# Kernel optimization log

Hardware: AMD Instinct MI355X
Metric: run time of the kernel (lower is better)

## Reference

```python
import jax, jax.numpy as jnp
import numpy as np

N, S, IN_F, TEXT_D, EMB, H = 128, 1024, 768, 512, 512, 8
HD = EMB // H  # 64


def setup_inputs() -> dict:
    key = jax.random.key(0)
    ks = jax.random.split(key, 14)
    sc = 0.02
    return {
        "v": jax.random.normal(ks[0], (1, N, 12, IN_F), dtype=jnp.float32),
        "t": jax.random.normal(ks[1], (N, S, TEXT_D), dtype=jnp.float32),
        "t_len": jax.random.randint(ks[2], (N,), 1, S + 1, dtype=jnp.int32),
        "W_fc1": jax.random.normal(ks[3], (EMB, IN_F), dtype=jnp.float32) * sc,
        "b_fc1": jnp.zeros((EMB,), jnp.float32),
        "W_fc2": jax.random.normal(ks[4], (EMB, 12 * EMB), dtype=jnp.float32) * sc,
        "b_fc2": jnp.zeros((EMB,), jnp.float32),
        "Wq": jax.random.normal(ks[5], (EMB, EMB), dtype=jnp.float32) * sc,
        "Wk": jax.random.normal(ks[6], (EMB, TEXT_D), dtype=jnp.float32) * sc,
        "Wv": jax.random.normal(ks[7], (EMB, TEXT_D), dtype=jnp.float32) * sc,
        "bq": jnp.zeros((EMB,), jnp.float32),
        "bk": jnp.zeros((EMB,), jnp.float32),
        "bv": jnp.zeros((EMB,), jnp.float32),
        "Wo": jax.random.normal(ks[8], (EMB, EMB), dtype=jnp.float32) * sc,
        "bo": jnp.zeros((EMB,), jnp.float32),
    }


def reference(v, t, t_len, W_fc1, b_fc1, W_fc2, b_fc2, Wq, Wk, Wv, bq, bk, bv, Wo, bo):
    # fc1 + ReLU: [1,N,12,IN_F] -> [N,12,EMB]
    x = jax.nn.relu(jnp.einsum('onif,ef->onie', v, W_fc1) + b_fc1)[0]
    # flatten + fc2 + ReLU -> [N, EMB]
    x = x.reshape(N, 12 * EMB)
    vfeat = jax.nn.relu(x @ W_fc2.T + b_fc2)
    # Batched ragged multihead attention, query length 1 per item.
    scale = 1.0 / jnp.sqrt(jnp.asarray(HD, vfeat.dtype))
    q = ((vfeat @ Wq.T + bq) * scale).reshape(N, H, HD)           # [N,H,HD]
    k = (jnp.einsum('nsd,ed->nse', t, Wk) + bk).reshape(N, S, H, HD)
    vv = (jnp.einsum('nsd,ed->nse', t, Wv) + bv).reshape(N, S, H, HD)
    scores = jnp.einsum('nhd,nshd->nhs', q, k)                    # [N,H,S]
    valid = (jnp.arange(S)[None, :] < t_len[:, None])[:, None, :]  # [N,1,S]
    scores = jnp.where(valid, scores, jnp.finfo(scores.dtype).min)
    w = jax.nn.softmax(scores, axis=-1)                           # [N,H,S]
    ctx = jnp.einsum('nhs,nshd->nhd', w, vv).reshape(N, EMB)
    attn_out = ctx @ Wo.T + bo                                    # [N,EMB]
    return vfeat, attn_out
```

## Files before the change

kernel.cpp:

```cpp
#include <hip/hip_runtime.h>

#define NB 128
#define SSEQ 1024
#define TD 512

typedef _Float16 half8 __attribute__((ext_vector_type(8)));
typedef _Float16 half4 __attribute__((ext_vector_type(4)));
typedef _Float16 half2v __attribute__((ext_vector_type(2)));
typedef float f32x4 __attribute__((ext_vector_type(4)));
typedef float f32x2 __attribute__((ext_vector_type(2)));

template<int AM, int BM>
__global__ __launch_bounds__(256) void k_gemm(
    const void* __restrict__ Av, int lda, long aSZ,
    const void* __restrict__ Bv, int ldb, long bSZ,
    const float* __restrict__ bias, const float* __restrict__ aRowScale,
    float scale, int doRelu, int outMode,
    float* __restrict__ outF, _Float16* __restrict__ outH,
    int ldc, int cColOff, int mtiles, int kTiles, long oSplit)
{
  __shared__ _Float16 As[64][72];
  __shared__ _Float16 Bs[64][72];
  int mt = blockIdx.x % mtiles, nt = blockIdx.x / mtiles;
  int sp = blockIdx.y, bz = blockIdx.z;
  int tid = threadIdx.x;
  int r = tid >> 2, kq = (tid & 3) * 16;
  int w = tid >> 6, l = tid & 63;
  long aoff = (long)bz * aSZ + (long)(mt * 64 + r) * lda + (long)sp * kTiles * 64 + kq;
  long boff = (long)bz * bSZ + (long)(nt * 64 + r) * ldb + (long)sp * kTiles * 64 + kq;
  const _Float16* apH = (const _Float16*)Av + aoff;
  const float*    apF = (const float*)Av + aoff;
  const _Float16* bpH = (const _Float16*)Bv + boff;
  const float*    bpF = (const float*)Bv + boff;
  float srA = 1.0f;
  if constexpr (AM == 2) srA = 1.0f / aRowScale[(mt * 64 + r) * 8 + bz];

  half8 pa0, pa1, pb0, pb1;
  f32x4 qa0, qa1, qa2, qa3, qc0, qc1, qc2, qc3;
  if constexpr (AM == 0) { pa0 = *(const half8*)apH; pa1 = *(const half8*)(apH + 8); }
  else { qa0 = *(const f32x4*)apF; qa1 = *(const f32x4*)(apF + 4);
         qa2 = *(const f32x4*)(apF + 8); qa3 = *(const f32x4*)(apF + 12); }
  if constexpr (BM == 0) { pb0 = *(const half8*)bpH; pb1 = *(const half8*)(bpH + 8); }
  else { qc0 = *(const f32x4*)bpF; qc1 = *(const f32x4*)(bpF + 4);
         qc2 = *(const f32x4*)(bpF + 8); qc3 = *(const f32x4*)(bpF + 12); }

  f32x4 acc[4];
  #pragma unroll
  for (int c = 0; c < 4; ++c) acc[c] = (f32x4){0.f, 0.f, 0.f, 0.f};
  int fr = l & 15, fo = (l >> 4) * 8;
  for (int kt = 0; kt < kTiles; ++kt) {
    __syncthreads();
    if constexpr (AM == 0) {
      *(half8*)&As[r][kq] = pa0; *(half8*)&As[r][kq + 8] = pa1;
    } else {
      f32x4 s0 = qa0, s1 = qa1, s2 = qa2, s3 = qa3;
      if constexpr (AM == 2) { s0 *= srA; s1 *= srA; s2 *= srA; s3 *= srA; }
      *(half4*)&As[r][kq + 0]  = __builtin_convertvector(s0, half4);
      *(half4*)&As[r][kq + 4]  = __builtin_convertvector(s1, half4);
      *(half4*)&As[r][kq + 8]  = __builtin_convertvector(s2, half4);
      *(half4*)&As[r][kq + 12] = __builtin_convertvector(s3, half4);
    }
    if constexpr (BM == 0) {
      *(half8*)&Bs[r][kq] = pb0; *(half8*)&Bs[r][kq + 8] = pb1;
    } else {
      *(half4*)&Bs[r][kq + 0]  = __builtin_convertvector(qc0, half4);
      *(half4*)&Bs[r][kq + 4]  = __builtin_convertvector(qc1, half4);
      *(half4*)&Bs[r][kq + 8]  = __builtin_convertvector(qc2, half4);
      *(half4*)&Bs[r][kq + 12] = __builtin_convertvector(qc3, half4);
    }
    __syncthreads();
    if (kt + 1 < kTiles) {
      apH += 64; apF += 64; bpH += 64; bpF += 64;
      if constexpr (AM == 0) { pa0 = *(const half8*)apH; pa1 = *(const half8*)(apH + 8); }
      else { qa0 = *(const f32x4*)apF; qa1 = *(const f32x4*)(apF + 4);
             qa2 = *(const f32x4*)(apF + 8); qa3 = *(const f32x4*)(apF + 12); }
      if constexpr (BM == 0) { pb0 = *(const half8*)bpH; pb1 = *(const half8*)(bpH + 8); }
      else { qc0 = *(const f32x4*)bpF; qc1 = *(const f32x4*)(bpF + 4);
             qc2 = *(const f32x4*)(bpF + 8); qc3 = *(const f32x4*)(bpF + 12); }
    }
    #pragma unroll
    for (int ks = 0; ks < 2; ++ks) {
      half8 af = *(const half8*)&As[16 * w + fr][ks * 32 + fo];
      #pragma unroll
      for (int c = 0; c < 4; ++c) {
        half8 bf = *(const half8*)&Bs[16 * c + fr][ks * 32 + fo];
        acc[c] = __builtin_amdgcn_mfma_f32_16x16x32_f16(af, bf, acc[c], 0, 0, 0);
      }
    }
  }
  int lrow = (l >> 4) * 4, lcol = l & 15;
  #pragma unroll
  for (int c = 0; c < 4; ++c) {
    #pragma unroll
    for (int rr = 0; rr < 4; ++rr) {
      int gm = mt * 64 + 16 * w + lrow + rr;
      int gn = nt * 64 + 16 * c + lcol;
      int ecol = gn + bz * cColOff;
      float vv = acc[c][rr];
      if (bias) vv += bias[ecol];
      vv *= scale;
      if (doRelu) vv = fmaxf(vv, 0.f);
      long oidx = (long)gm * ldc + ecol;
      if (outMode == 0) outF[oidx] = vv;
      else if (outMode == 1) outH[oidx] = (_Float16)vv;
      else outF[oidx + (long)sp * oSplit] = vv;
    }
  }
}

__global__ __launch_bounds__(256) void k_vfeat(
    const float* __restrict__ vacc, const float* __restrict__ b2,
    float* __restrict__ outF, _Float16* __restrict__ vf16)
{
  int i = blockIdx.x * 256 + threadIdx.x;
  float vv = b2[i & 511];
  #pragma unroll
  for (int sp = 0; sp < 16; ++sp) vv += vacc[sp * 65536 + i];
  vv = fmaxf(vv, 0.f);
  outF[i] = vv;
  vf16[i] = (_Float16)vv;
}

__global__ __launch_bounds__(256) void k_qk(
    const float* __restrict__ qf, const float* __restrict__ Wk,
    const float* __restrict__ bk, _Float16* __restrict__ qk16, float* __restrict__ qb)
{
  int n = blockIdx.x, tid = threadIdx.x;
  __shared__ float qs[512];
  qs[tid] = qf[n * 512 + tid];
  qs[tid + 256] = qf[n * 512 + tid + 256];
  __syncthreads();
  _Float16* qn = qk16 + (long)n * 8192;
  #pragma unroll 1
  for (int h = 0; h < 8; ++h) {
    float a0 = 0.f, a1 = 0.f;
    #pragma unroll 8
    for (int j = 0; j < 64; ++j) {
      float qv = qs[h * 64 + j];
      const float* wr = Wk + (long)(h * 64 + j) * 512;
      a0 = fmaf(qv, wr[tid], a0);
      a1 = fmaf(qv, wr[tid + 256], a1);
    }
    qn[h * 512 + tid] = (_Float16)a0;
    qn[h * 512 + tid + 256] = (_Float16)a1;
  }
  #pragma unroll
  for (int h = 8; h < 16; ++h) {
    qn[h * 512 + tid] = (_Float16)0.f;
    qn[h * 512 + tid + 256] = (_Float16)0.f;
  }
  if (tid < 64) {
    #pragma unroll 1
    for (int h = 0; h < 8; ++h) {
      float pb = qs[h * 64 + tid] * bk[h * 64 + tid];
      #pragma unroll
      for (int m = 1; m < 64; m <<= 1) pb += __shfl_xor(pb, m, 64);
      if (tid == 0) qb[n * 8 + h] = pb;
    }
  }
}

__global__ __launch_bounds__(256) void k_attn(
    const float* __restrict__ t, const int* __restrict__ tlen,
    const _Float16* __restrict__ qk16, const float* __restrict__ qb,
    float* __restrict__ pu, float* __restrict__ pl)
{
  int n = blockIdx.x >> 5, j = blockIdx.x & 31;
  int len = tlen[n];
  int base = j * 32;
  if (base >= len) return;
  int s1 = base + 32; if (s1 > len) s1 = len;
  int tid = threadIdx.x, wid = tid >> 6, l = tid & 63;

  __shared__ __align__(16) _Float16 ts[32][520];
  __shared__ __align__(16) float ws[32][8];
  __shared__ float lred[8];
  if (tid < 8) lred[tid] = 0.f;

  const float* tn = t + (long)n * SSEQ * TD;
  {
    f32x4 a0, a1, b0, b1;
    auto ld = [&](int c, f32x4& x0, f32x4& x1) {
      int sg = base + c * 4 + wid;
      if (sg < s1) {
        const float* p = tn + (long)sg * TD;
        x0 = *(const f32x4*)(p + 4 * l);
        x1 = *(const f32x4*)(p + 256 + 4 * l);
      } else {
        x0 = (f32x4){0.f,0.f,0.f,0.f}; x1 = (f32x4){0.f,0.f,0.f,0.f};
      }
    };
    ld(0, a0, a1); ld(1, b0, b1);
    #pragma unroll
    for (int c = 0; c < 8; c += 2) {
      half4 h0 = __builtin_convertvector(a0, half4);
      half4 h1 = __builtin_convertvector(a1, half4);
      int row = c * 4 + wid;
      if (c + 2 < 8) ld(c + 2, a0, a1);
      *(half4*)&ts[row][4 * l] = h0;
      *(half4*)&ts[row][256 + 4 * l] = h1;
      half4 g0 = __builtin_convertvector(b0, half4);
      half4 g1 = __builtin_convertvector(b1, half4);
      int row2 = c * 4 + 4 + wid;
      if (c + 3 < 8) ld(c + 3, b0, b1);
      *(half4*)&ts[row2][4 * l] = g0;
      *(half4*)&ts[row2][256 + 4 * l] = g1;
    }
  }
  __syncthreads();
  int fr = l & 15, fo = (l >> 4) * 8;
  if (wid < 2) {
    const _Float16* qn = qk16 + (long)n * 8192 + fr * 512 + fo;
    f32x4 acc = (f32x4){0.f, 0.f, 0.f, 0.f};
    #pragma unroll 4
    for (int kt = 0; kt < 16; ++kt) {
      half8 bf = *(const half8*)(qn + kt * 32);
      half8 af = *(const half8*)&ts[16 * wid + fr][kt * 32 + fo];
      acc = __builtin_amdgcn_mfma_f32_16x16x32_f16(af, bf, acc, 0, 0, 0);
    }
    float qbr = (fr < 8) ? qb[n * 8 + fr] : 0.f;
    float lac = 0.f;
    #pragma unroll
    for (int r = 0; r < 4; ++r) {
      int sl = 16 * wid + (l >> 4) * 4 + r;
      float wv = 0.f;
      if (fr < 8 && base + sl < s1) wv = __expf(acc[r] + qbr);
      if (fr < 8) ws[sl][fr] = wv;
      lac += wv;
    }
    if (fr < 8) atomicAdd(&lred[fr], lac);
  }
  __syncthreads();
  int col0 = 128 * wid + 2 * l;
  f32x2 u[8];
  #pragma unroll
  for (int h = 0; h < 8; ++h) u[h] = (f32x2){0.f, 0.f};
  #pragma unroll 4
  for (int r = 0; r < 32; ++r) {
    f32x4 wa = *(const f32x4*)&ws[r][0];
    f32x4 wb = *(const f32x4*)&ws[r][4];
    half2v tv = *(const half2v*)&ts[r][col0];
    f32x2 tp = { (float)tv[0], (float)tv[1] };
    u[0] += wa[0] * tp; u[1] += wa[1] * tp;
    u[2] += wa[2] * tp; u[3] += wa[3] * tp;
    u[4] += wb[0] * tp; u[5] += wb[1] * tp;
    u[6] += wb[2] * tp; u[7] += wb[3] * tp;
  }
  float* pn = pu + (long)n * 4096;
  #pragma unroll
  for (int h = 0; h < 8; ++h) {
    atomicAdd(&pn[h * 512 + col0], u[h][0]);
    atomicAdd(&pn[h * 512 + col0 + 1], u[h][1]);
  }
  if (tid < 8) atomicAdd(&pl[n * 8 + tid], lred[tid]);
}

extern "C" void kernel_launch(void* const* d_in, const int* in_sizes, int n_in,
                              void* d_out, int out_size, void* d_ws, size_t ws_size,
                              hipStream_t stream)
{
  const float* v    = (const float*)d_in[0];
  const float* t    = (const float*)d_in[1];
  const int*   tlen = (const int*)d_in[2];
  const float* W1   = (const float*)d_in[3];
  const float* b1   = (const float*)d_in[4];
  const float* W2   = (const float*)d_in[5];
  const float* b2   = (const float*)d_in[6];
  const float* Wq   = (const float*)d_in[7];
  const float* Wk   = (const float*)d_in[8];
  const float* Wv   = (const float*)d_in[9];
  const float* bq   = (const float*)d_in[10];
  const float* bk   = (const float*)d_in[11];
  const float* bv   = (const float*)d_in[12];
  const float* Wo   = (const float*)d_in[13];
  const float* bo   = (const float*)d_in[14];
  float* out = (float*)d_out;

  _Float16* hb   = (_Float16*)d_ws;
  _Float16* x16  = hb;
  _Float16* vf16 = hb + 786432l;
  _Float16* ctx16= hb + 851968l;
  _Float16* qk16 = hb + 917504l;
  float* fb   = (float*)(hb + 1966080l);
  float* vacc = fb;
  float* qf   = fb + 1048576l;
  float* pu   = fb + 1114112l;
  float* pl   = fb + 1638400l;
  float* qb   = fb + 1639424l;

  hipMemsetAsync(pu, 0, (524288l + 1024l) * sizeof(float), stream);
  k_gemm<1,1><<<dim3(192, 1, 1), 256, 0, stream>>>(v, 768, 0, W1, 768, 0,
      b1, nullptr, 1.f, 1, 1, nullptr, x16, 512, 0, 24, 12, 0);
  k_gemm<0,1><<<dim3(16, 16, 1), 256, 0, stream>>>(x16, 6144, 0, W2, 6144, 0,
      nullptr, nullptr, 1.f, 0, 2, vacc, nullptr, 512, 0, 2, 6, 65536);
  k_vfeat<<<256, 256, 0, stream>>>(vacc, b2, out, vf16);
  k_gemm<0,1><<<dim3(16, 1, 1), 256, 0, stream>>>(vf16, 512, 0, Wq, 512, 0,
      bq, nullptr, 0.125f, 0, 0, qf, nullptr, 512, 0, 2, 8, 0);
  k_qk<<<128, 256, 0, stream>>>(qf, Wk, bk, qk16, qb);
  k_attn<<<NB * 32, 256, 0, stream>>>(t, tlen, qk16, qb, pu, pl);
  k_gemm<2,1><<<dim3(2, 1, 8), 256, 0, stream>>>(pu, 4096, 512, Wv, 512, 32768,
      bv, pl, 1.f, 0, 1, nullptr, ctx16, 512, 64, 2, 8, 0);
  k_gemm<0,1><<<dim3(16, 1, 1), 256, 0, stream>>>(ctx16, 512, 0, Wo, 512, 0,
      bo, nullptr, 1.f, 0, 0, out + 65536, nullptr, 512, 0, 2, 8, 0);
}
```

Measured before the change: 518.9 us.

## Use MFMA for weighted-sum in attention and process two chunks per block

The attention kernel now handles 64 sequence positions per block in two 32-row sub-chunks, keeping per-block partial sums in registers across both chunks. The scalar FMA accumulation of exp-weights times text rows is replaced with a 16x16x32 f16 MFMA, with the weights stored as fp16 in a transposed shared buffer. This halves the global atomic flushes per sequence position and moves the weighted-sum work onto matrix cores. The trade-offs are fewer blocks, an extra barrier per chunk, strided column gathers from shared memory to build the B fragments, and lower precision because the weights are stored in fp16.

```diff
diff --git a/kernel.cpp b/kernel.cpp
--- a/kernel.cpp
+++ b/kernel.cpp
@@ -6,9 +6,7 @@
 
 typedef _Float16 half8 __attribute__((ext_vector_type(8)));
 typedef _Float16 half4 __attribute__((ext_vector_type(4)));
-typedef _Float16 half2v __attribute__((ext_vector_type(2)));
 typedef float f32x4 __attribute__((ext_vector_type(4)));
-typedef float f32x2 __attribute__((ext_vector_type(2)));
 
 template<int AM, int BM>
 __global__ __launch_bounds__(256) void k_gemm(
@@ -165,92 +163,103 @@
     const _Float16* __restrict__ qk16, const float* __restrict__ qb,
     float* __restrict__ pu, float* __restrict__ pl)
 {
-  int n = blockIdx.x >> 5, j = blockIdx.x & 31;
+  int n = blockIdx.x >> 4, j = blockIdx.x & 15;
   int len = tlen[n];
-  int base = j * 32;
-  if (base >= len) return;
-  int s1 = base + 32; if (s1 > len) s1 = len;
+  int base0 = j * 64;
+  if (base0 >= len) return;
   int tid = threadIdx.x, wid = tid >> 6, l = tid & 63;
+  int fr = l & 15, fo = (l >> 4) * 8;
 
   __shared__ __align__(16) _Float16 ts[32][520];
-  __shared__ __align__(16) float ws[32][8];
+  __shared__ __align__(16) _Float16 wst[16][32];
   __shared__ float lred[8];
   if (tid < 8) lred[tid] = 0.f;
 
   const float* tn = t + (long)n * SSEQ * TD;
-  {
-    f32x4 a0, a1, b0, b1;
-    auto ld = [&](int c, f32x4& x0, f32x4& x1) {
-      int sg = base + c * 4 + wid;
-      if (sg < s1) {
-        const float* p = tn + (long)sg * TD;
-        x0 = *(const f32x4*)(p + 4 * l);
-        x1 = *(const f32x4*)(p + 256 + 4 * l);
-      } else {
-        x0 = (f32x4){0.f,0.f,0.f,0.f}; x1 = (f32x4){0.f,0.f,0.f,0.f};
-      }
-    };
-    ld(0, a0, a1); ld(1, b0, b1);
+  const _Float16* qn = qk16 + (long)n * 8192 + fr * 512 + fo;
+  float qbr = (fr < 8) ? qb[n * 8 + fr] : 0.f;
+
+  f32x4 upv[8];
+  #pragma unroll
+  for (int dt = 0; dt < 8; ++dt) upv[dt] = (f32x4){0.f, 0.f, 0.f, 0.f};
+
+  #pragma unroll 1
+  for (int sub = 0; sub < 2; ++sub) {
+    int base = base0 + sub * 32;
+    if (base >= len) break;
+    int s1 = base + 32; if (s1 > len) s1 = len;
+    __syncthreads();
+    {
+      f32x4 a0, a1, b0, b1;
+      auto ld = [&](int c, f32x4& x0, f32x4& x1) {
+        int sg = base + c * 4 + wid;
+        if (sg < s1) {
+          const float* p = tn + (long)sg * TD;
+          x0 = *(const f32x4*)(p + 4 * l);
+          x1 = *(const f32x4*)(p + 256 + 4 * l);
+        } else {
+          x0 = (f32x4){0.f,0.f,0.f,0.f}; x1 = (f32x4){0.f,0.f,0.f,0.f};
+        }
+      };
+      ld(0, a0, a1); ld(1, b0, b1);
+      #pragma unroll
+      for (int c = 0; c < 8; c += 2) {
+        half4 h0 = __builtin_convertvector(a0, half4);
+        half4 h1 = __builtin_convertvector(a1, half4);
+        int row = c * 4 + wid;
+        if (c + 2 < 8) ld(c + 2, a0, a1);
+        *(half4*)&ts[row][4 * l] = h0;
+        *(half4*)&ts[row][256 + 4 * l] = h1;
+        half4 g0 = __builtin_convertvector(b0, half4);
+        half4 g1 = __builtin_convertvector(b1, half4);
+        int row2 = c * 4 + 4 + wid;
+        if (c + 3 < 8) ld(c + 3, b0, b1);
+        *(half4*)&ts[row2][4 * l] = g0;
+        *(half4*)&ts[row2][256 + 4 * l] = g1;
+      }
+    }
+    __syncthreads();
+    if (wid < 2) {
+      f32x4 acc = (f32x4){0.f, 0.f, 0.f, 0.f};
+      #pragma unroll 4
+      for (int kt = 0; kt < 16; ++kt) {
+        half8 bf = *(const half8*)(qn + kt * 32);
+        half8 af = *(const half8*)&ts[16 * wid + fr][kt * 32 + fo];
+        acc = __builtin_amdgcn_mfma_f32_16x16x32_f16(af, bf, acc, 0, 0, 0);
+      }
+      float lac = 0.f;
+      #pragma unroll
+      for (int r = 0; r < 4; ++r) {
+        int sl = 16 * wid + (l >> 4) * 4 + r;
+        float wv = (fr < 8 && base + sl < s1) ? __expf(acc[r] + qbr) : 0.f;
+        wst[fr][sl] = (_Float16)wv;
+        lac += wv;
+      }
+      if (fr < 8) atomicAdd(&lred[fr], lac);
+    }
+    __syncthreads();
+    {
+      half8 af = *(const half8*)&wst[fr][fo];
+      #pragma unroll
+      for (int dt = 0; dt < 8; ++dt) {
+        int dcol = 128 * wid + dt * 16 + fr;
+        half8 bf;
+        #pragma unroll
+        for (int jj = 0; jj < 8; ++jj) bf[jj] = ts[fo + jj][dcol];
+        upv[dt] = __builtin_amdgcn_mfma_f32_16x16x32_f16(af, bf, upv[dt], 0, 0, 0);
+      }
+    }
+  }
+  int quad = l >> 4;
+  float* pn = pu + (long)n * 4096;
+  if (quad < 2) {
     #pragma unroll
-    for (int c = 0; c < 8; c += 2) {
-      half4 h0 = __builtin_convertvector(a0, half4);
-      half4 h1 = __builtin_convertvector(a1, half4);
-      int row = c * 4 + wid;
-      if (c + 2 < 8) ld(c + 2, a0, a1);
-      *(half4*)&ts[row][4 * l] = h0;
-      *(half4*)&ts[row][256 + 4 * l] = h1;
-      half4 g0 = __builtin_convertvector(b0, half4);
-      half4 g1 = __builtin_convertvector(b1, half4);
-      int row2 = c * 4 + 4 + wid;
-      if (c + 3 < 8) ld(c + 3, b0, b1);
-      *(half4*)&ts[row2][4 * l] = g0;
-      *(half4*)&ts[row2][256 + 4 * l] = g1;
-    }
-  }
-  __syncthreads();
-  int fr = l & 15, fo = (l >> 4) * 8;
-  if (wid < 2) {
-    const _Float16* qn = qk16 + (long)n * 8192 + fr * 512 + fo;
-    f32x4 acc = (f32x4){0.f, 0.f, 0.f, 0.f};
-    #pragma unroll 4
-    for (int kt = 0; kt < 16; ++kt) {
-      half8 bf = *(const half8*)(qn + kt * 32);
-      half8 af = *(const half8*)&ts[16 * wid + fr][kt * 32 + fo];
-      acc = __builtin_amdgcn_mfma_f32_16x16x32_f16(af, bf, acc, 0, 0, 0);
-    }
-    float qbr = (fr < 8) ? qb[n * 8 + fr] : 0.f;
-    float lac = 0.f;
-    #pragma unroll
-    for (int r = 0; r < 4; ++r) {
-      int sl = 16 * wid + (l >> 4) * 4 + r;
-      float wv = 0.f;
-      if (fr < 8 && base + sl < s1) wv = __expf(acc[r] + qbr);
-      if (fr < 8) ws[sl][fr] = wv;
-      lac += wv;
-    }
-    if (fr < 8) atomicAdd(&lred[fr], lac);
-  }
-  __syncthreads();
-  int col0 = 128 * wid + 2 * l;
-  f32x2 u[8];
-  #pragma unroll
-  for (int h = 0; h < 8; ++h) u[h] = (f32x2){0.f, 0.f};
-  #pragma unroll 4
-  for (int r = 0; r < 32; ++r) {
-    f32x4 wa = *(const f32x4*)&ws[r][0];
-    f32x4 wb = *(const f32x4*)&ws[r][4];
-    half2v tv = *(const half2v*)&ts[r][col0];
-    f32x2 tp = { (float)tv[0], (float)tv[1] };
-    u[0] += wa[0] * tp; u[1] += wa[1] * tp;
-    u[2] += wa[2] * tp; u[3] += wa[3] * tp;
-    u[4] += wb[0] * tp; u[5] += wb[1] * tp;
-    u[6] += wb[2] * tp; u[7] += wb[3] * tp;
-  }
-  float* pn = pu + (long)n * 4096;
-  #pragma unroll
-  for (int h = 0; h < 8; ++h) {
-    atomicAdd(&pn[h * 512 + col0], u[h][0]);
-    atomicAdd(&pn[h * 512 + col0 + 1], u[h][1]);
+    for (int dt = 0; dt < 8; ++dt) {
+      int d = 128 * wid + dt * 16 + fr;
+      #pragma unroll
+      for (int r = 0; r < 4; ++r)
+        atomicAdd(&pn[(quad * 4 + r) * 512 + d], upv[dt][r]);
+    }
   }
   if (tid < 8) atomicAdd(&pl[n * 8 + tid], lred[tid]);
 }
@@ -297,7 +306,7 @@
   k_gemm<0,1><<<dim3(16, 1, 1), 256, 0, stream>>>(vf16, 512, 0, Wq, 512, 0,
       bq, nullptr, 0.125f, 0, 0, qf, nullptr, 512, 0, 2, 8, 0);
   k_qk<<<128, 256, 0, stream>>>(qf, Wk, bk, qk16, qb);
-  k_attn<<<NB * 32, 256, 0, stream>>>(t, tlen, qk16, qb, pu, pl);
+  k_attn<<<NB * 16, 256, 0, stream>>>(t, tlen, qk16, qb, pu, pl);
   k_gemm<2,1><<<dim3(2, 1, 8), 256, 0, stream>>>(pu, 4096, 512, Wv, 512, 32768,
       bv, pl, 1.f, 0, 1, nullptr, ctx16, 512, 64, 2, 8, 0);
   k_gemm<0,1><<<dim3(16, 1, 1), 256, 0, stream>>>(ctx16, 512, 0, Wo, 512, 0,
```

Result: faster. 491.3 us (-5.3%).
